# Optimization experiments

Hardware: AMD Instinct MI355X
Metric: run time of the kernel (lower is better)

Reference implementation:

```python
import jax, jax.numpy as jnp
import numpy as np

N_NODES = 50000
N_HYPEREDGES = 50000
E = 320000
D = 256


def _prelu(x, a):
    return jnp.where(x >= 0, x, a * x)


def _hypergraph_conv(x, hei, W, b, num_nodes, num_edges):
    # PyG HypergraphConv, use_attention=False, heads=1:
    # out = D^{-1} H B^{-1} H^T (X W^T) + b
    src = hei[0]  # node indices, [E]
    he = hei[1]   # hyperedge indices, [E]
    xw = x @ W.T  # [N, D] node transform (lin has no bias)
    ones = jnp.ones((hei.shape[1],), x.dtype)
    deg_n = jax.ops.segment_sum(ones, src, num_segments=num_nodes)   # node degree D
    deg_e = jax.ops.segment_sum(ones, he, num_segments=num_edges)    # hyperedge size B
    d_inv = jnp.where(deg_n > 0, 1.0 / deg_n, 0.0)
    b_inv = jnp.where(deg_e > 0, 1.0 / deg_e, 0.0)
    # node -> hyperedge aggregation, scaled by B^{-1}
    edge_feat = b_inv[:, None] * jax.ops.segment_sum(xw[src], he, num_segments=num_edges)  # [n_he, D]
    # hyperedge -> node aggregation, scaled by D^{-1}
    out = d_inv[:, None] * jax.ops.segment_sum(edge_feat[he], src, num_segments=num_nodes)  # [N, D]
    return out + b


def setup_inputs() -> dict:
    key = jax.random.key(0)
    ks = jax.random.split(key, 6)
    std = np.sqrt(2.0 / D)  # kaiming_normal
    x = jax.random.normal(ks[0], (N_NODES, D), dtype=jnp.float32)
    hyper_edge_index = jax.random.randint(ks[1], (2, E), 0, N_HYPEREDGES, dtype=jnp.int64)
    W1 = jax.random.normal(ks[2], (D, D), dtype=jnp.float32) * std
    b1 = jnp.zeros((D,), jnp.float32)
    W2 = jax.random.normal(ks[3], (D, D), dtype=jnp.float32) * std
    b2 = jnp.zeros((D,), jnp.float32)
    prelu_a = jnp.asarray(0.25, jnp.float32)
    return {"x": x, "W1": W1, "b1": b1, "W2": W2, "b2": b2,
            "prelu_a": prelu_a, "hyper_edge_index": hyper_edge_index}


def reference(x, W1, b1, W2, b2, prelu_a, hyper_edge_index):
    out = _hypergraph_conv(x, hyper_edge_index, W1, b1, N_NODES, N_HYPEREDGES)
    out = _prelu(out, prelu_a)
    out = _hypergraph_conv(out, hyper_edge_index, W2, b2, N_NODES, N_HYPEREDGES)
    out = out + x  # residual
    out = _prelu(out, prelu_a)
    return out
```

## Files before the change

kernel.cpp:

```cpp
#include <hip/hip_runtime.h>

#define NN    50000
#define NHE   50000
#define NEDGE 320000
#define DD    256

#define SB    1024
#define NBLK  ((NN + SB - 1) / SB)

typedef float f32x4 __attribute__((ext_vector_type(4)));
typedef short short8 __attribute__((ext_vector_type(8)));

static __device__ __forceinline__ unsigned short f2b(float f) {
    union { float f; unsigned u; } c; c.f = f;
    unsigned u = c.u;
    u += 0x7fffu + ((u >> 16) & 1u);
    return (unsigned short)(u >> 16);
}
static __device__ __forceinline__ float b2f_lo(unsigned v) {
    union { unsigned u; float f; } c; c.u = v << 16; return c.f;
}
static __device__ __forceinline__ float b2f_hi(unsigned v) {
    union { unsigned u; float f; } c; c.u = v & 0xffff0000u; return c.f;
}
static __device__ __forceinline__ unsigned pack2(float a, float b) {
    return (unsigned)f2b(a) | ((unsigned)f2b(b) << 16);
}

__global__ __launch_bounds__(256) void k_count(const int* __restrict__ src,
                                               const int* __restrict__ he,
                                               int* __restrict__ cnt_n,
                                               int* __restrict__ cnt_e) {
    int e = blockIdx.x * 256 + threadIdx.x;
    if (e >= NEDGE) return;
    atomicAdd(&cnt_n[src[e]], 1);
    atomicAdd(&cnt_e[he[e]], 1);
}

__global__ __launch_bounds__(256) void k_scan_a(const int* __restrict__ cnt_n,
                                                const int* __restrict__ cnt_e,
                                                int* __restrict__ bsum) {
    int b   = blockIdx.x;
    int seg = b / NBLK, lb = b % NBLK;
    const int* cnt = seg ? cnt_e : cnt_n;
    int t = threadIdx.x;
    int idx = lb * SB + t * 4;
    int s = 0;
#pragma unroll
    for (int j = 0; j < 4; ++j)
        if (idx + j < NN) s += cnt[idx + j];
    __shared__ int red[256];
    red[t] = s;
    __syncthreads();
    for (int o = 128; o > 0; o >>= 1) {
        if (t < o) red[t] += red[t + o];
        __syncthreads();
    }
    if (t == 0) bsum[b] = red[0];
}

__global__ __launch_bounds__(64) void k_scan_b(const int* __restrict__ bsum,
                                               int* __restrict__ bbase) {
    if (threadIdx.x == 0) {
        int r = 0;
        for (int i = 0; i < NBLK; ++i) { bbase[i] = r; r += bsum[i]; }
        bbase[2 * NBLK] = r;
        r = 0;
        for (int i = NBLK; i < 2 * NBLK; ++i) { bbase[i] = r; r += bsum[i]; }
        bbase[2 * NBLK + 1] = r;
    }
}

__global__ __launch_bounds__(256) void k_scan_c(const int* __restrict__ cnt_n,
                                                const int* __restrict__ cnt_e,
                                                const int* __restrict__ bbase,
                                                int* __restrict__ off_n,
                                                int* __restrict__ off_e) {
    int b   = blockIdx.x;
    int seg = b / NBLK, lb = b % NBLK;
    const int* cnt = seg ? cnt_e : cnt_n;
    int* off = seg ? off_e : off_n;
    int t = threadIdx.x;
    int idx = lb * SB + t * 4;
    int v[4];
    int tsum = 0;
#pragma unroll
    for (int j = 0; j < 4; ++j) {
        v[j] = (idx + j < NN) ? cnt[idx + j] : 0;
        tsum += v[j];
    }
    __shared__ int sc[256];
    sc[t] = tsum;
    __syncthreads();
    for (int o = 1; o < 256; o <<= 1) {
        int val = (t >= o) ? sc[t - o] : 0;
        __syncthreads();
        sc[t] += val;
        __syncthreads();
    }
    int p = bbase[b] + sc[t] - tsum;
#pragma unroll
    for (int j = 0; j < 4; ++j) {
        if (idx + j < NN) off[idx + j] = p;
        p += v[j];
    }
    if (b == 0 && t == 0) off_n[NN] = bbase[2 * NBLK];
    if (b == NBLK && t == 0) off_e[NHE] = bbase[2 * NBLK + 1];
}

__global__ __launch_bounds__(256) void k_fill(const int* __restrict__ src,
                                              const int* __restrict__ he,
                                              const int* __restrict__ off_n,
                                              const int* __restrict__ off_e,
                                              int* __restrict__ cur_n,
                                              int* __restrict__ cur_e,
                                              int* __restrict__ adj_n,
                                              int* __restrict__ adj_e) {
    int e = blockIdx.x * 256 + threadIdx.x;
    if (e >= NEDGE) return;
    int s = src[e], h = he[e];
    int pn = off_n[s] + atomicAdd(&cur_n[s], 1);
    adj_n[pn] = h;
    int pe = off_e[h] + atomicAdd(&cur_e[h], 1);
    adj_e[pe] = s;
}

__global__ __launch_bounds__(256) void k_cvt_w(const float* __restrict__ w1,
                                               const float* __restrict__ w2,
                                               unsigned short* __restrict__ o1,
                                               unsigned short* __restrict__ o2) {
    int t = blockIdx.x * 256 + threadIdx.x;
    const int n4 = DD * DD / 4;
    const float* s = (t < n4) ? w1 : w2;
    unsigned short* d = (t < n4) ? o1 : o2;
    int i = (t < n4) ? t : t - n4;
    float4 v = ((const float4*)s)[i];
    uint2 o;
    o.x = pack2(v.x, v.y);
    o.y = pack2(v.z, v.w);
    ((uint2*)d)[i] = o;
}

template <bool A32>
__global__ __launch_bounds__(256) void k_gemm_bf16(const void* __restrict__ Av,
                                                   const unsigned short* __restrict__ Wb,
                                                   unsigned short* __restrict__ Cb, int M) {
    __shared__ __align__(16) unsigned short As[64 * 32];
    __shared__ __align__(16) unsigned short Bs[128 * 32];
    const int t    = threadIdx.x;
    const int m0   = blockIdx.x * 64;
    const int n0   = blockIdx.y * 128;
    const int lane = t & 63;
    const int wave = t >> 6;
    const int wm   = (wave >> 1) * 32;
    const int wn   = (wave & 1) * 64;
    const int fr   = lane & 15;
    const int fq   = lane >> 4;

    f32x4 acc[2][4] = {};

    const int sr = t >> 2;
    const int ss = t & 3;

    for (int k0 = 0; k0 < DD; k0 += 32) {
        uint4 av = make_uint4(0u, 0u, 0u, 0u);
        {
            int gm = m0 + sr;
            if (gm < M) {
                if (A32) {
                    const float* p = (const float*)Av + (size_t)gm * DD + k0 + ss * 8;
                    float4 f0 = *(const float4*)p;
                    float4 f1 = *(const float4*)(p + 4);
                    av.x = pack2(f0.x, f0.y);
                    av.y = pack2(f0.z, f0.w);
                    av.z = pack2(f1.x, f1.y);
                    av.w = pack2(f1.z, f1.w);
                } else {
                    av = *(const uint4*)((const unsigned short*)Av + (size_t)gm * DD + k0 + ss * 8);
                }
            }
        }
        uint4 bv0 = *(const uint4*)(Wb + (size_t)(n0 + sr) * DD + k0 + ss * 8);
        uint4 bv1 = *(const uint4*)(Wb + (size_t)(n0 + sr + 64) * DD + k0 + ss * 8);
        __syncthreads();
        *(uint4*)(As + sr * 32 + ((ss ^ (sr & 3)) * 8)) = av;
        {
            int r0 = sr, r1 = sr + 64;
            *(uint4*)(Bs + r0 * 32 + ((ss ^ (r0 & 3)) * 8)) = bv0;
            *(uint4*)(Bs + r1 * 32 + ((ss ^ (r1 & 3)) * 8)) = bv1;
        }
        __syncthreads();

        short8 af[2], bf[4];
#pragma unroll
        for (int mt = 0; mt < 2; ++mt) {
            int r = wm + mt * 16 + fr;
            af[mt] = *(const short8*)(As + r * 32 + ((fq ^ (r & 3)) * 8));
        }
#pragma unroll
        for (int nt = 0; nt < 4; ++nt) {
            int r = wn + nt * 16 + fr;
            bf[nt] = *(const short8*)(Bs + r * 32 + ((fq ^ (r & 3)) * 8));
        }
#pragma unroll
        for (int mt = 0; mt < 2; ++mt)
#pragma unroll
            for (int nt = 0; nt < 4; ++nt)
                acc[mt][nt] = __builtin_amdgcn_mfma_f32_16x16x32_bf16(af[mt], bf[nt],
                                                                      acc[mt][nt], 0, 0, 0);
    }

#pragma unroll
    for (int mt = 0; mt < 2; ++mt) {
#pragma unroll
        for (int i = 0; i < 4; ++i) {
            int gm = m0 + wm + mt * 16 + fq * 4 + i;
            if (gm >= M) continue;
#pragma unroll
            for (int nt = 0; nt < 4; ++nt) {
                int gn = n0 + wn + nt * 16 + fr;
                Cb[(size_t)gm * DD + gn] = f2b(acc[mt][nt][i]);
            }
        }
    }
}

static __device__ __forceinline__ void acc8(float* a, uint4 v) {
    a[0] += b2f_lo(v.x); a[1] += b2f_hi(v.x);
    a[2] += b2f_lo(v.y); a[3] += b2f_hi(v.y);
    a[4] += b2f_lo(v.z); a[5] += b2f_hi(v.z);
    a[6] += b2f_lo(v.w); a[7] += b2f_hi(v.w);
}
static __device__ __forceinline__ void gather8(const unsigned short* __restrict__ srcb,
                                               const int* __restrict__ adj,
                                               int b, int e, int sl, float* a) {
#pragma unroll
    for (int i = 0; i < 8; ++i) a[i] = 0.f;
    for (int i = b; i < e; i += 8) {
        int g0 = adj[i];
        int g[8];
        g[0] = g0;
#pragma unroll
        for (int j = 1; j < 8; ++j) g[j] = (i + j < e) ? adj[i + j] : g0;
        uint4 v[8];
#pragma unroll
        for (int j = 0; j < 8; ++j)
            v[j] = *(const uint4*)(srcb + (size_t)g[j] * DD + sl * 8);
        acc8(a, v[0]);
#pragma unroll
        for (int j = 1; j < 8; ++j)
            if (i + j < e) acc8(a, v[j]);
    }
}

__global__ __launch_bounds__(256) void k_gather_edge_b(const unsigned short* __restrict__ xw,
                                                       unsigned short* __restrict__ ef,
                                                       const int* __restrict__ off,
                                                       const int* __restrict__ adj) {
    int tid = blockIdx.x * 256 + threadIdx.x;
    int w = tid >> 5;
    int sl = tid & 31;
    if (w >= NHE) return;
    int b = off[w], e = off[w + 1];
    float a[8];
    gather8(xw, adj, b, e, sl, a);
    float sc = (e > b) ? 1.f / (float)(e - b) : 0.f;
    uint4 o;
    o.x = pack2(a[0] * sc, a[1] * sc);
    o.y = pack2(a[2] * sc, a[3] * sc);
    o.z = pack2(a[4] * sc, a[5] * sc);
    o.w = pack2(a[6] * sc, a[7] * sc);
    *(uint4*)(ef + (size_t)w * DD + sl * 8) = o;
}

__global__ __launch_bounds__(256) void k_gather_node_mid_b(const unsigned short* __restrict__ ef,
                                                           unsigned short* __restrict__ h,
                                                           const int* __restrict__ off,
                                                           const int* __restrict__ adj,
                                                           const float* __restrict__ bias,
                                                           const float* __restrict__ aP) {
    int tid = blockIdx.x * 256 + threadIdx.x;
    int w = tid >> 5;
    int sl = tid & 31;
    if (w >= NN) return;
    int b = off[w], e = off[w + 1];
    float a[8];
    gather8(ef, adj, b, e, sl, a);
    float sc = (e > b) ? 1.f / (float)(e - b) : 0.f;
    float al = *aP;
    float4 bb0 = ((const float4*)bias)[sl * 2];
    float4 bb1 = ((const float4*)bias)[sl * 2 + 1];
    float r[8];
    r[0] = a[0] * sc + bb0.x; r[1] = a[1] * sc + bb0.y;
    r[2] = a[2] * sc + bb0.z; r[3] = a[3] * sc + bb0.w;
    r[4] = a[4] * sc + bb1.x; r[5] = a[5] * sc + bb1.y;
    r[6] = a[6] * sc + bb1.z; r[7] = a[7] * sc + bb1.w;
#pragma unroll
    for (int i = 0; i < 8; ++i) r[i] = (r[i] >= 0.f) ? r[i] : al * r[i];
    uint4 o;
    o.x = pack2(r[0], r[1]);
    o.y = pack2(r[2], r[3]);
    o.z = pack2(r[4], r[5]);
    o.w = pack2(r[6], r[7]);
    *(uint4*)(h + (size_t)w * DD + sl * 8) = o;
}

__global__ __launch_bounds__(256) void k_gather_node_final_b(const unsigned short* __restrict__ ef,
                                                             const float* __restrict__ x,
                                                             float* __restrict__ out,
                                                             const int* __restrict__ off,
                                                             const int* __restrict__ adj,
                                                             const float* __restrict__ bias,
                                                             const float* __restrict__ aP) {
    int tid = blockIdx.x * 256 + threadIdx.x;
    int w = tid >> 5;
    int sl = tid & 31;
    if (w >= NN) return;
    int b = off[w], e = off[w + 1];
    float a[8];
    gather8(ef, adj, b, e, sl, a);
    float sc = (e > b) ? 1.f / (float)(e - b) : 0.f;
    float al = *aP;
    float4 bb0 = ((const float4*)bias)[sl * 2];
    float4 bb1 = ((const float4*)bias)[sl * 2 + 1];
    const float* xp = x + (size_t)w * DD + sl * 8;
    float4 xv0 = *(const float4*)xp;
    float4 xv1 = *(const float4*)(xp + 4);
    float r[8];
    r[0] = a[0] * sc + bb0.x + xv0.x; r[1] = a[1] * sc + bb0.y + xv0.y;
    r[2] = a[2] * sc + bb0.z + xv0.z; r[3] = a[3] * sc + bb0.w + xv0.w;
    r[4] = a[4] * sc + bb1.x + xv1.x; r[5] = a[5] * sc + bb1.y + xv1.y;
    r[6] = a[6] * sc + bb1.z + xv1.z; r[7] = a[7] * sc + bb1.w + xv1.w;
#pragma unroll
    for (int i = 0; i < 8; ++i) r[i] = (r[i] >= 0.f) ? r[i] : al * r[i];
    float* op = out + (size_t)w * DD + sl * 8;
    *(float4*)op = make_float4(r[0], r[1], r[2], r[3]);
    *(float4*)(op + 4) = make_float4(r[4], r[5], r[6], r[7]);
}

extern "C" void kernel_launch(void* const* d_in, const int* in_sizes, int n_in,
                              void* d_out, int out_size, void* d_ws, size_t ws_size,
                              hipStream_t stream) {
    const float* x       = (const float*)d_in[0];
    const float* W1      = (const float*)d_in[1];
    const float* b1      = (const float*)d_in[2];
    const float* W2      = (const float*)d_in[3];
    const float* b2      = (const float*)d_in[4];
    const float* prelu_a = (const float*)d_in[5];
    const int*   hei     = (const int*)d_in[6];
    const int* idx_src = hei;
    const int* idx_he  = hei + NEDGE;

    float* out = (float*)d_out;
    unsigned short* B1 = (unsigned short*)d_ws;
    unsigned short* B2 = B1 + (size_t)NN * DD;
    int* off_n = (int*)(B2 + (size_t)NN * DD);
    int* off_e = off_n + NN + 1;
    int* cur_n = off_e + NHE + 1;
    int* cur_e = cur_n + NN;
    int* adj_n = cur_e + NHE;
    int* adj_e = adj_n + NEDGE;
    int* bsum  = adj_e + NEDGE;
    int* bbase = bsum + 2 * NBLK;
    unsigned short* w1b = (unsigned short*)d_out;
    unsigned short* w2b = w1b + DD * DD;

    const int eblocks = (NEDGE + 255) / 256;
    const int gblocks = (NN * 32 + 255) / 256;
    dim3 ggrid((NN + 63) / 64, DD / 128);

    hipMemsetAsync(cur_n, 0, sizeof(int) * (NN + NHE), stream);
    k_count<<<eblocks, 256, 0, stream>>>(idx_src, idx_he, cur_n, cur_e);
    k_scan_a<<<2 * NBLK, 256, 0, stream>>>(cur_n, cur_e, bsum);
    k_scan_b<<<1, 64, 0, stream>>>(bsum, bbase);
    k_scan_c<<<2 * NBLK, 256, 0, stream>>>(cur_n, cur_e, bbase, off_n, off_e);
    hipMemsetAsync(cur_n, 0, sizeof(int) * (NN + NHE), stream);
    k_fill<<<eblocks, 256, 0, stream>>>(idx_src, idx_he, off_n, off_e,
                                        cur_n, cur_e, adj_n, adj_e);

    k_cvt_w<<<(2 * DD * DD / 4 + 255) / 256, 256, 0, stream>>>(W1, W2, w1b, w2b);

    k_gemm_bf16<true><<<ggrid, 256, 0, stream>>>((const void*)x, w1b, B1, NN);
    k_gather_edge_b<<<gblocks, 256, 0, stream>>>(B1, B2, off_e, adj_e);
    k_gather_node_mid_b<<<gblocks, 256, 0, stream>>>(B2, B1, off_n, adj_n, b1, prelu_a);

    k_gemm_bf16<false><<<ggrid, 256, 0, stream>>>((const void*)B1, w2b, B2, NN);
    k_gather_edge_b<<<gblocks, 256, 0, stream>>>(B2, B1, off_e, adj_e);
    k_gather_node_final_b<<<gblocks, 256, 0, stream>>>(B1, x, out, off_n, adj_n, b2, prelu_a);
}
```

Baseline: 339.3 us.

## Enlarge GEMM tile to 128x128 with direct global-to-LDS loads and fold memset

Doubles the GEMM M-tile to 128 rows so each wave computes 4x4 MFMA tiles, raising reuse of the weight tile. Weight tiles, and bf16 activations in the second layer, now go straight from global memory into LDS through global_load_lds, skipping the register staging. The second memset of the cursor arrays is dropped; the scan kernel zeroes them instead. The costs are more accumulator registers per thread and the new direct-to-LDS path, which has to keep the same swizzled layout.

```diff
diff --git a/kernel.cpp b/kernel.cpp
--- a/kernel.cpp
+++ b/kernel.cpp
@@ -25,6 +25,12 @@
 }
 static __device__ __forceinline__ unsigned pack2(float a, float b) {
     return (unsigned)f2b(a) | ((unsigned)f2b(b) << 16);
+}
+
+static __device__ __forceinline__ void glds16(const unsigned short* g, unsigned short* l) {
+    __builtin_amdgcn_global_load_lds((const __attribute__((address_space(1))) unsigned int*)g,
+                                     (__attribute__((address_space(3))) unsigned int*)l,
+                                     16, 0, 0);
 }
 
 __global__ __launch_bounds__(256) void k_count(const int* __restrict__ src,
@@ -75,11 +81,14 @@
                                                 const int* __restrict__ cnt_e,
                                                 const int* __restrict__ bbase,
                                                 int* __restrict__ off_n,
-                                                int* __restrict__ off_e) {
+                                                int* __restrict__ off_e,
+                                                int* __restrict__ cur_n,
+                                                int* __restrict__ cur_e) {
     int b   = blockIdx.x;
     int seg = b / NBLK, lb = b % NBLK;
     const int* cnt = seg ? cnt_e : cnt_n;
     int* off = seg ? off_e : off_n;
+    int* cur = seg ? cur_e : cur_n;
     int t = threadIdx.x;
     int idx = lb * SB + t * 4;
     int v[4];
@@ -101,7 +110,7 @@
     int p = bbase[b] + sc[t] - tsum;
 #pragma unroll
     for (int j = 0; j < 4; ++j) {
-        if (idx + j < NN) off[idx + j] = p;
+        if (idx + j < NN) { off[idx + j] = p; cur[idx + j] = 0; }
         p += v[j];
     }
     if (b == 0 && t == 0) off_n[NN] = bbase[2 * NBLK];
@@ -142,58 +151,67 @@
 }
 
 template <bool A32>
-__global__ __launch_bounds__(256) void k_gemm_bf16(const void* __restrict__ Av,
-                                                   const unsigned short* __restrict__ Wb,
-                                                   unsigned short* __restrict__ Cb, int M) {
-    __shared__ __align__(16) unsigned short As[64 * 32];
+__global__ __launch_bounds__(256) void k_gemm128(const void* __restrict__ Av,
+                                                 const unsigned short* __restrict__ Wb,
+                                                 unsigned short* __restrict__ Cb, int M) {
+    __shared__ __align__(16) unsigned short As[128 * 32];
     __shared__ __align__(16) unsigned short Bs[128 * 32];
     const int t    = threadIdx.x;
-    const int m0   = blockIdx.x * 64;
+    const int m0   = blockIdx.x * 128;
     const int n0   = blockIdx.y * 128;
     const int lane = t & 63;
     const int wave = t >> 6;
-    const int wm   = (wave >> 1) * 32;
+    const int wm   = (wave >> 1) * 64;
     const int wn   = (wave & 1) * 64;
     const int fr   = lane & 15;
     const int fq   = lane >> 4;
 
-    f32x4 acc[2][4] = {};
-
-    const int sr = t >> 2;
-    const int ss = t & 3;
+    f32x4 acc[4][4] = {};
+
+    const int rl0 = wave * 32 + (lane >> 2);
+    const int ar = t >> 1;
+    const int ah = t & 1;
 
     for (int k0 = 0; k0 < DD; k0 += 32) {
-        uint4 av = make_uint4(0u, 0u, 0u, 0u);
-        {
-            int gm = m0 + sr;
-            if (gm < M) {
-                if (A32) {
-                    const float* p = (const float*)Av + (size_t)gm * DD + k0 + ss * 8;
-                    float4 f0 = *(const float4*)p;
-                    float4 f1 = *(const float4*)(p + 4);
-                    av.x = pack2(f0.x, f0.y);
-                    av.y = pack2(f0.z, f0.w);
-                    av.z = pack2(f1.x, f1.y);
-                    av.w = pack2(f1.z, f1.w);
-                } else {
-                    av = *(const uint4*)((const unsigned short*)Av + (size_t)gm * DD + k0 + ss * 8);
-                }
+        __syncthreads();
+#pragma unroll
+        for (int q = 0; q < 2; ++q) {
+            int rl = rl0 + q * 16;
+            int c  = (lane & 3) ^ (rl & 3);
+            glds16(Wb + (size_t)(n0 + rl) * DD + k0 + c * 8,
+                   Bs + (size_t)(wave * 32 + q * 16) * 32);
+        }
+        if (A32) {
+            int gr = m0 + ar; if (gr >= M) gr = M - 1;
+            const float* p = (const float*)Av + (size_t)gr * DD + k0 + ah * 16;
+            float4 f0 = ((const float4*)p)[0];
+            float4 f1 = ((const float4*)p)[1];
+            float4 f2 = ((const float4*)p)[2];
+            float4 f3 = ((const float4*)p)[3];
+            uint4 u0, u1;
+            u0.x = pack2(f0.x, f0.y); u0.y = pack2(f0.z, f0.w);
+            u0.z = pack2(f1.x, f1.y); u0.w = pack2(f1.z, f1.w);
+            u1.x = pack2(f2.x, f2.y); u1.y = pack2(f2.z, f2.w);
+            u1.z = pack2(f3.x, f3.y); u1.w = pack2(f3.z, f3.w);
+            int p0 = (2 * ah) ^ (ar & 3);
+            int p1 = (2 * ah + 1) ^ (ar & 3);
+            *(uint4*)(As + ar * 32 + p0 * 8) = u0;
+            *(uint4*)(As + ar * 32 + p1 * 8) = u1;
+        } else {
+#pragma unroll
+            for (int q = 0; q < 2; ++q) {
+                int rl = rl0 + q * 16;
+                int gr = m0 + rl; if (gr >= M) gr = M - 1;
+                int c  = (lane & 3) ^ (rl & 3);
+                glds16((const unsigned short*)Av + (size_t)gr * DD + k0 + c * 8,
+                       As + (size_t)(wave * 32 + q * 16) * 32);
             }
         }
-        uint4 bv0 = *(const uint4*)(Wb + (size_t)(n0 + sr) * DD + k0 + ss * 8);
-        uint4 bv1 = *(const uint4*)(Wb + (size_t)(n0 + sr + 64) * DD + k0 + ss * 8);
         __syncthreads();
-        *(uint4*)(As + sr * 32 + ((ss ^ (sr & 3)) * 8)) = av;
-        {
-            int r0 = sr, r1 = sr + 64;
-            *(uint4*)(Bs + r0 * 32 + ((ss ^ (r0 & 3)) * 8)) = bv0;
-            *(uint4*)(Bs + r1 * 32 + ((ss ^ (r1 & 3)) * 8)) = bv1;
-        }
-        __syncthreads();
-
-        short8 af[2], bf[4];
-#pragma unroll
-        for (int mt = 0; mt < 2; ++mt) {
+
+        short8 af[4], bf[4];
+#pragma unroll
+        for (int mt = 0; mt < 4; ++mt) {
             int r = wm + mt * 16 + fr;
             af[mt] = *(const short8*)(As + r * 32 + ((fq ^ (r & 3)) * 8));
         }
@@ -203,7 +221,7 @@
             bf[nt] = *(const short8*)(Bs + r * 32 + ((fq ^ (r & 3)) * 8));
         }
 #pragma unroll
-        for (int mt = 0; mt < 2; ++mt)
+        for (int mt = 0; mt < 4; ++mt)
 #pragma unroll
             for (int nt = 0; nt < 4; ++nt)
                 acc[mt][nt] = __builtin_amdgcn_mfma_f32_16x16x32_bf16(af[mt], bf[nt],
@@ -211,7 +229,7 @@
     }
 
 #pragma unroll
-    for (int mt = 0; mt < 2; ++mt) {
+    for (int mt = 0; mt < 4; ++mt) {
 #pragma unroll
         for (int i = 0; i < 4; ++i) {
             int gm = m0 + wm + mt * 16 + fq * 4 + i;
@@ -367,24 +385,24 @@
 
     const int eblocks = (NEDGE + 255) / 256;
     const int gblocks = (NN * 32 + 255) / 256;
-    dim3 ggrid((NN + 63) / 64, DD / 128);
+    dim3 ggrid((NN + 127) / 128, DD / 128);
 
     hipMemsetAsync(cur_n, 0, sizeof(int) * (NN + NHE), stream);
     k_count<<<eblocks, 256, 0, stream>>>(idx_src, idx_he, cur_n, cur_e);
     k_scan_a<<<2 * NBLK, 256, 0, stream>>>(cur_n, cur_e, bsum);
     k_scan_b<<<1, 64, 0, stream>>>(bsum, bbase);
-    k_scan_c<<<2 * NBLK, 256, 0, stream>>>(cur_n, cur_e, bbase, off_n, off_e);
-    hipMemsetAsync(cur_n, 0, sizeof(int) * (NN + NHE), stream);
+    k_scan_c<<<2 * NBLK, 256, 0, stream>>>(cur_n, cur_e, bbase, off_n, off_e,
+                                           cur_n, cur_e);
     k_fill<<<eblocks, 256, 0, stream>>>(idx_src, idx_he, off_n, off_e,
                                         cur_n, cur_e, adj_n, adj_e);
 
     k_cvt_w<<<(2 * DD * DD / 4 + 255) / 256, 256, 0, stream>>>(W1, W2, w1b, w2b);
 
-    k_gemm_bf16<true><<<ggrid, 256, 0, stream>>>((const void*)x, w1b, B1, NN);
+    k_gemm128<true><<<ggrid, 256, 0, stream>>>((const void*)x, w1b, B1, NN);
     k_gather_edge_b<<<gblocks, 256, 0, stream>>>(B1, B2, off_e, adj_e);
     k_gather_node_mid_b<<<gblocks, 256, 0, stream>>>(B2, B1, off_n, adj_n, b1, prelu_a);
 
-    k_gemm_bf16<false><<<ggrid, 256, 0, stream>>>((const void*)B1, w2b, B2, NN);
+    k_gemm128<false><<<ggrid, 256, 0, stream>>>((const void*)B1, w2b, B2, NN);
     k_gather_edge_b<<<gblocks, 256, 0, stream>>>(B2, B1, off_e, adj_e);
     k_gather_node_final_b<<<gblocks, 256, 0, stream>>>(B1, x, out, off_n, adj_n, b2, prelu_a);
 }
```

Result: no change. 335.6 us (-1.1%).
